# Kernel optimization log

Measured on AMD Instinct MI355X. Metric: run time of the kernel, lower is better.

The kernel has to match this reference:

```python
import jax, jax.numpy as jnp
import numpy as np
from jax.ops import segment_sum, segment_max

N, D, B = 1536, 32, 8            # nodes, candidate out-degree per node, sequential batch steps
OBS, HID, HEADS, C = 33, 64, 4, 8  # obs_dim, GRU hidden, attn heads, out_dim//heads
E = N * D


def setup_inputs() -> dict:
    key = jax.random.key(0)
    ks = jax.random.split(key, 16)
    g = lambda i, shape, s=0.1: jax.random.normal(ks[i], shape, jnp.float32) * s
    src = jnp.repeat(jnp.arange(N), D)                    # uniform degree -> scatter_topk = row top-k
    dst = jax.random.randint(ks[0], (E,), 0, N)
    return dict(
        H_t=jax.random.normal(ks[1], (B, N, OBS), jnp.float32),
        src=src, dst=dst, k=4,
        W_e1=g(2, (OBS, 32)), b_e1=jnp.zeros(32), W_e2=g(3, (32, 32)), b_e2=jnp.zeros(32),
        ln_g=jnp.ones(32), ln_b=jnp.zeros(32),
        W_ih=g(4, (3 * HID, 32)), W_hh=g(5, (3 * HID, HID)),
        b_ih=jnp.zeros(3 * HID), b_hh=jnp.zeros(3 * HID),
        W_s1=g(6, (2 * HID, 64)), b_s1=jnp.zeros(64), W_s2=g(7, (64, 1)), b_s2=jnp.zeros(1),
        W_gat=g(8, (HID, HEADS * C)), att_src=g(9, (HEADS, C)), att_dst=g(10, (HEADS, C)),
        b_gat=jnp.zeros(HEADS * C),
    )


def _layernorm(x, g, b, eps=1e-5):
    mu = x.mean(-1, keepdims=True)
    var = ((x - mu) ** 2).mean(-1, keepdims=True)
    return (x - mu) * jax.lax.rsqrt(var + eps) * g + b


def _forward(H_t, src, dst, k, W_e1, b_e1, W_e2, b_e2, ln_g, ln_b,
             W_ih, W_hh, b_ih, b_hh, W_s1, b_s1, W_s2, b_s2,
             W_gat, att_src, att_dst, b_gat):
    # ObsEmbedding: Linear-ReLU-Linear-ReLU-LayerNorm, applied to all (B,N) at once
    x = jax.nn.relu(H_t @ W_e1 + b_e1)
    x = jax.nn.relu(x @ W_e2 + b_e2)
    H_emb = _layernorm(x, ln_g, ln_b)              # (B,N,32)

    def step(h, e_t):
        # --- NodeMemory: shared GRUCell, h carried across batch steps ---
        gi = e_t @ W_ih.T + b_ih                   # (N,3H)
        gh = h @ W_hh.T + b_hh
        i_r, i_z, i_n = jnp.split(gi, 3, -1)
        h_r, h_z, h_n = jnp.split(gh, 3, -1)
        r = jax.nn.sigmoid(i_r + h_r)
        z = jax.nn.sigmoid(i_z + h_z)
        n = jnp.tanh(i_n + r * h_n)
        h_new = (1.0 - z) * n + z * h              # (N,HID)

        # --- EdgeScorer: sigmoid MLP score per candidate edge, keep top-k per source ---
        feat = jnp.concatenate([h_new[src], h_new[dst]], -1)        # (E,2*HID)
        score = jax.nn.sigmoid(
            (jax.nn.relu(feat @ W_s1 + b_s1) @ W_s2 + b_s2)[:, 0])  # (E,)
        s2 = score.reshape(N, D)
        top_idx = jax.lax.top_k(s2, k)[1]                           # (N,k)
        keep = (jnp.zeros((N, D), bool)
                .at[jnp.arange(N)[:, None], top_idx].set(True)).reshape(-1)  # (E,)
        w = jnp.where(keep, score, 0.0)                             # soft edge weights

        # --- GATConv (add_self_loops=False), pruned edges masked out of the softmax ---
        xh = (h_new @ W_gat).reshape(N, HEADS, C)
        a_s = (xh * att_src).sum(-1)               # (N,HEADS)
        a_d = (xh * att_dst).sum(-1)
        logit = jax.nn.leaky_relu(a_s[src] + a_d[dst], 0.2)         # (E,HEADS)
        logit = jnp.where(keep[:, None], logit, -1e30)
        m = segment_max(logit, dst, num_segments=N)                 # softmax grouped by target
        ex = jnp.where(keep[:, None], jnp.exp(logit - m[dst]), 0.0)
        ssum = segment_sum(ex, dst, num_segments=N)
        alpha = ex / jnp.clip(ssum[dst], 1e-16)                     # (E,HEADS)

        msg = alpha[:, :, None] * xh[src] * w[:, None, None]        # edge_weight scales messages
        out = segment_sum(msg, dst, num_segments=N).reshape(N, HEADS * C) + b_gat

        # --- densify attention: scatter-accumulate then row-normalize ---
        A = jnp.zeros((HEADS, N, N), alpha.dtype).at[:, src, dst].add(alpha.T)
        A = A / jnp.clip(A.sum(-1, keepdims=True), 1e-9)
        return h_new, (out, A)

    h0 = jnp.zeros((N, HID), H_t.dtype)
    _, (outs, attns) = jax.lax.scan(step, h0, H_emb)
    return outs, attns                              # (B,N,32), (B,HEADS,N,N)


def reference(H_t, src, dst, k, W_e1, b_e1, W_e2, b_e2, ln_g, ln_b,
              W_ih, W_hh, b_ih, b_hh, W_s1, b_s1, W_s2, b_s2,
              W_gat, att_src, att_dst, b_gat):
    return _forward(H_t, src, dst, k, W_e1, b_e1, W_e2, b_e2, ln_g, ln_b,
                    W_ih, W_hh, b_ih, b_hh, W_s1, b_s1, W_s2, b_s2,
                    W_gat, att_src, att_dst, b_gat)
```

## Files before the change

### kernel.cpp

```cpp
#include <hip/hip_runtime.h>
#include <math.h>

#define NN   1536
#define DG   32
#define BB   8
#define OBSD 33
#define HID  64
#define NHEAD 4
#define EE   (NN*DG)

__device__ __forceinline__ float sigm(float x){ return 1.0f/(1.0f+expf(-x)); }

__global__ void __launch_bounds__(256) k_embgi(
                      const float* __restrict__ Ht,
                      const float* __restrict__ We1, const float* __restrict__ be1,
                      const float* __restrict__ We2, const float* __restrict__ be2,
                      const float* __restrict__ lng, const float* __restrict__ lnb,
                      const float* __restrict__ Wih, const float* __restrict__ bih,
                      float* __restrict__ GI, int* __restrict__ cursor){
    __shared__ float lwih[192*33];
    int tid = threadIdx.x;
    if(blockIdx.x < 6) cursor[blockIdx.x*256 + tid] = 0;
    for(int i=tid;i<192*32;i+=256){ int r=i>>5, c=i&31; lwih[r*33+c]=Wih[i]; }
    __syncthreads();
    int lane = tid & 63;
    int j32 = lane & 31;
    int bn = blockIdx.x*4 + (tid>>6);
    const float* hrow = Ht + (size_t)bn*OBSD;
    float x1 = be1[j32];
    for(int o=0;o<OBSD;o++) x1 += hrow[o]*We1[o*32+j32];
    x1 = fmaxf(x1,0.f);
    float x2 = be2[j32];
    for(int i=0;i<32;i++){
        float xi = __shfl(x1, (lane & 32) | i, 64);
        x2 += xi * We2[i*32+j32];
    }
    x2 = fmaxf(x2,0.f);
    float mu = x2;
    for(int m=16;m>=1;m>>=1) mu += __shfl_xor(mu, m, 32);
    mu *= (1.0f/32.0f);
    float d = x2-mu; float var = d*d;
    for(int m=16;m>=1;m>>=1) var += __shfl_xor(var, m, 32);
    var *= (1.0f/32.0f);
    float xln = d*rsqrtf(var+1e-5f)*lng[j32]+lnb[j32];
    int j = lane;
    float gr=bih[j], gz=bih[64+j], gn=bih[128+j];
    for(int kk=0;kk<32;kk++){
        float ek = __shfl(xln, kk, 64);
        gr += ek*lwih[j*33+kk];
        gz += ek*lwih[(64+j)*33+kk];
        gn += ek*lwih[(128+j)*33+kk];
    }
    float* g = GI + (size_t)bn*192;
    g[j]=gr; g[64+j]=gz; g[128+j]=gn;
}

__global__ void k_count(const int* __restrict__ dst, int* __restrict__ cursor){
    int e = blockIdx.x*256+threadIdx.x;
    if(e<EE) atomicAdd(&cursor[dst[e]],1);
}
__global__ void k_scan(int* __restrict__ cnt, int* __restrict__ indptr){
    __shared__ int part[256];
    int t = threadIdx.x;
    int local[6]; int s=0;
    for(int i=0;i<6;i++){ local[i]=cnt[t*6+i]; s+=local[i]; }
    part[t]=s; __syncthreads();
    if(t==0){ int acc=0; for(int i=0;i<256;i++){ int v=part[i]; part[i]=acc; acc+=v; } }
    __syncthreads();
    int pre = part[t];
    for(int i=0;i<6;i++){ int idx=t*6+i; indptr[idx]=pre; cnt[idx]=pre; pre+=local[i]; }
    if(t==255) indptr[NN]=EE;
}
__global__ void k_fill(const int* __restrict__ dst, int* __restrict__ cursor, int* __restrict__ eids){
    int e = blockIdx.x*256+threadIdx.x;
    if(e<EE){ int p = atomicAdd(&cursor[dst[e]],1); eids[p]=e; }
}

__global__ void __launch_bounds__(384) k_gru_all(const float* __restrict__ GI,
                       const float* __restrict__ Whh, const float* __restrict__ bhh,
                       float* __restrict__ Hall){
    __shared__ float lw[192*65];
    int tid = threadIdx.x;
    for(int i=tid;i<192*64;i+=384){ int r=i>>6, c=i&63; lw[r*65+c]=Whh[i]; }
    __syncthreads();
    int node = blockIdx.x*6 + (tid>>6);
    int j = tid&63;
    float rw[64], rz[64], rn[64];
    #pragma unroll
    for(int kk=0;kk<64;kk++){
        rw[kk]=lw[j*65+kk];
        rz[kk]=lw[(64+j)*65+kk];
        rn[kk]=lw[(128+j)*65+kk];
    }
    float b_r=bhh[j], b_z=bhh[64+j], b_n=bhh[128+j];
    float hold = 0.f;
    for(int t=0;t<BB;t++){
        float hr=b_r, hz=b_z, hn=b_n;
        #pragma unroll
        for(int kk=0;kk<64;kk++){
            float hk = __shfl(hold,kk);
            hr += hk*rw[kk];
            hz += hk*rz[kk];
            hn += hk*rn[kk];
        }
        const float* g = GI + ((size_t)t*NN+node)*192;
        float r  = sigm(g[j]     + hr);
        float z  = sigm(g[64+j]  + hz);
        float nn_= tanhf(g[128+j] + r*hn);
        hold = (1.f-z)*nn_ + z*hold;
        Hall[((size_t)t*NN+node)*64 + j] = hold;
    }
}

__global__ void __launch_bounds__(256) k_post(const float* __restrict__ Hall,
                       const float* __restrict__ Ws1, const float* __restrict__ Wgat,
                       const float* __restrict__ atts, const float* __restrict__ attd,
                       float* __restrict__ P, float* __restrict__ Q,
                       float* __restrict__ xh, float* __restrict__ as_, float* __restrict__ ad_){
    __shared__ float ws1l[128*64];
    __shared__ float wgl[64*32];
    int tid = threadIdx.x;
    for(int i=tid;i<128*64;i+=256) ws1l[i]=Ws1[i];
    for(int i=tid;i<64*32;i+=256)  wgl[i]=Wgat[i];
    __syncthreads();
    int bn = blockIdx.x*4 + (tid>>6);
    int j = tid&63;
    float hv = Hall[(size_t)bn*64+j];
    float p=0.f,q=0.f,xv=0.f;
    for(int kk=0;kk<64;kk++){
        float hk=__shfl(hv,kk);
        p += hk*ws1l[kk*64+j];
        q += hk*ws1l[(64+kk)*64+j];
        if(j<32) xv += hk*wgl[kk*32+j];
    }
    P[(size_t)bn*64+j]=p; Q[(size_t)bn*64+j]=q;
    if(j<32){
        xh[(size_t)bn*32+j]=xv;
        float asv = xv*atts[j];
        float adv = xv*attd[j];
        for(int m=1;m<8;m<<=1){ asv += __shfl_xor(asv,m); adv += __shfl_xor(adv,m); }
        if((j&7)==0){ as_[(size_t)bn*4+(j>>3)]=asv; ad_[(size_t)bn*4+(j>>3)]=adv; }
    }
}

__global__ void __launch_bounds__(256) k_edge(const float* __restrict__ P, const float* __restrict__ Q,
                       const float* __restrict__ bs1, const float* __restrict__ Ws2,
                       const float* __restrict__ bs2, const int* __restrict__ dst,
                       const int* __restrict__ kptr, float* __restrict__ wbuf){
    __shared__ float sc[DG];
    int tid = threadIdx.x;
    int t = blockIdx.y;
    int row = blockIdx.x;
    int wv = tid>>6, j = tid&63;
    float pv = P[((size_t)t*NN+row)*64 + j];
    float bv = bs1[j], w2 = Ws2[j];
    float b2 = bs2[0];
    int des[8];
    #pragma unroll
    for(int i=0;i<8;i++) des[i] = dst[row*DG + wv*8 + i];
    float qv[8];
    #pragma unroll
    for(int i=0;i<8;i++) qv[i] = Q[((size_t)t*NN+des[i])*64 + j];
    #pragma unroll
    for(int i=0;i<8;i++){
        float v = fmaxf(pv+qv[i]+bv,0.f)*w2;
        for(int m=32;m>=1;m>>=1) v += __shfl_xor(v,m);
        if(j==0) sc[wv*8+i] = sigm(v+b2);
    }
    __syncthreads();
    if(tid<32){
        float score = sc[tid];
        int kk = kptr[0]; if(kk>32) kk=32; if(kk<0) kk=0;
        bool sel=false;
        for(int it=0; it<kk; it++){
            float v = sel ? -INFINITY : score;
            int idx = tid;
            for(int m=16;m>=1;m>>=1){
                float ov = __shfl_xor(v,m,32);
                int   oi = __shfl_xor(idx,m,32);
                if(ov>v || (ov==v && oi<idx)){ v=ov; idx=oi; }
            }
            if(idx==tid) sel=true;
        }
        wbuf[(size_t)t*EE + row*DG + tid] = sel ? score : 0.f;
    }
}

__global__ void __launch_bounds__(256) k_soft(const int* __restrict__ indptr, const int* __restrict__ eids,
                       const float* __restrict__ as_, const float* __restrict__ ad_,
                       const float* __restrict__ wbuf, const float* __restrict__ xhb,
                       const float* __restrict__ bgat,
                       float* __restrict__ alphab, float* __restrict__ outp){
    int n = blockIdx.x;
    int t = blockIdx.y;
    int h = threadIdx.x>>6;
    int lane = threadIdx.x&63;
    const float* w     = wbuf  + (size_t)t*EE;
    const float* asb   = as_   + (size_t)t*NN*4;
    const float* xhbt  = xhb   + (size_t)t*NN*32;
    float*       alpha = alphab+ (size_t)t*EE*4;
    int beg = indptr[n], end = indptr[n+1];
    int deg = end-beg;
    float adv = ad_[((size_t)t*NN+n)*4+h];
    float acc[8];
    #pragma unroll
    for(int c=0;c<8;c++) acc[c]=0.f;
    if(deg<=64){
        bool valid = lane<deg;
        int e = valid ? eids[beg+lane] : 0;
        float we = valid ? w[e] : 0.f;
        bool kept = we>0.f;
        int s = e>>5;
        float lg = -INFINITY, ex = 0.f;
        if(kept){
            lg = asb[s*4+h]+adv;
            lg = lg>0.f ? lg : 0.2f*lg;
        }
        float m = lg;
        for(int mm=32;mm>=1;mm>>=1) m = fmaxf(m,__shfl_xor(m,mm));
        if(kept) ex = expf(lg-m);
        float ssum = ex;
        for(int mm=32;mm>=1;mm>>=1) ssum += __shfl_xor(ssum,mm);
        float inv = 1.0f/fmaxf(ssum,1e-16f);
        if(kept){
            float a = ex*inv;
            alpha[e*4+h] = a;
            float aw = a*we;
            const float4* xr = (const float4*)(xhbt + s*32 + h*8);
            float4 x0 = xr[0], x1 = xr[1];
            acc[0]+=aw*x0.x; acc[1]+=aw*x0.y; acc[2]+=aw*x0.z; acc[3]+=aw*x0.w;
            acc[4]+=aw*x1.x; acc[5]+=aw*x1.y; acc[6]+=aw*x1.z; acc[7]+=aw*x1.w;
        }
    } else {
        float m = -INFINITY;
        for(int i=beg+lane;i<end;i+=64){
            int e = eids[i];
            if(w[e]>0.f){
                float lg = asb[(e>>5)*4+h]+adv;
                lg = lg>0.f ? lg : 0.2f*lg;
                m = fmaxf(m,lg);
            }
        }
        for(int mm=32;mm>=1;mm>>=1) m = fmaxf(m,__shfl_xor(m,mm));
        float ssum=0.f;
        for(int i=beg+lane;i<end;i+=64){
            int e = eids[i];
            float ex = 0.f;
            if(w[e]>0.f){
                float lg = asb[(e>>5)*4+h]+adv;
                lg = lg>0.f ? lg : 0.2f*lg;
                ex = expf(lg-m);
            }
            alpha[e*4+h]=ex;
            ssum += ex;
        }
        for(int mm=32;mm>=1;mm>>=1) ssum += __shfl_xor(ssum,mm);
        float inv = 1.0f/fmaxf(ssum,1e-16f);
        for(int i=beg+lane;i<end;i+=64){
            int e = eids[i];
            if(w[e]>0.f){
                float a = alpha[e*4+h]*inv;
                alpha[e*4+h]=a;
                float aw = a*w[e];
                const float* xr = xhbt + (e>>5)*32 + h*8;
                #pragma unroll
                for(int c=0;c<8;c++) acc[c] += aw*xr[c];
            } 
        }
    }
    for(int mm=32;mm>=1;mm>>=1){
        #pragma unroll
        for(int c=0;c<8;c++) acc[c] += __shfl_xor(acc[c],mm);
    }
    if(lane==0){
        float* o = outp + ((size_t)t*NN+n)*32 + h*8;
        float4 o0 = { acc[0]+bgat[h*8+0], acc[1]+bgat[h*8+1], acc[2]+bgat[h*8+2], acc[3]+bgat[h*8+3] };
        float4 o1 = { acc[4]+bgat[h*8+4], acc[5]+bgat[h*8+5], acc[6]+bgat[h*8+6], acc[7]+bgat[h*8+7] };
        ((float4*)o)[0]=o0; ((float4*)o)[1]=o1;
    }
}

__global__ void __launch_bounds__(256) k_scatter(const float* __restrict__ alphab,
                       const float* __restrict__ wbuf,
                       const int* __restrict__ dst, float* __restrict__ attn){
    __shared__ int   kde[DG];
    __shared__ float kan[DG][NHEAD];
    __shared__ int   scnt;
    int n = blockIdx.x;
    int t = blockIdx.y;
    int tid = threadIdx.x;
    const float* alpha = alphab + (size_t)t*EE*4;
    const float* w     = wbuf   + (size_t)t*EE;
    if(tid<64){
        int d = tid;
        int e = n*DG + d;
        bool kept = false;
        if(d<DG) kept = (w[e] > 0.f);
        unsigned long long mask = __ballot(kept);
        float4 av = {0.f,0.f,0.f,0.f};
        int de = 0;
        if(kept){ de = dst[e]; av = *(const float4*)(alpha + (size_t)e*4); }
        float s0=av.x, s1=av.y, s2=av.z, s3=av.w;
        for(int m=32;m>=1;m>>=1){
            s0 += __shfl_xor(s0,m); s1 += __shfl_xor(s1,m);
            s2 += __shfl_xor(s2,m); s3 += __shfl_xor(s3,m);
        }
        if(kept){
            int pos = __popcll(mask & ((1ull<<d)-1ull));
            kde[pos] = de;
            kan[pos][0] = av.x / fmaxf(s0,1e-9f);
            kan[pos][1] = av.y / fmaxf(s1,1e-9f);
            kan[pos][2] = av.z / fmaxf(s2,1e-9f);
            kan[pos][3] = av.w / fmaxf(s3,1e-9f);
        }
        if(tid==0) scnt = __popcll(mask);
    }
    __syncthreads();
    int cnt = scnt;
    size_t base = (size_t)t*NHEAD*NN*NN + (size_t)n*NN;
    #pragma unroll
    for(int it=0; it<6; it++){
        int c = it*256 + tid;
        int h = c/(NN/4), c4 = c%(NN/4);
        float4 f4 = {0.f,0.f,0.f,0.f};
        for(int p=0;p<cnt;p++){
            int de = kde[p];
            if((de>>2)==c4) ((float*)&f4)[de&3] += kan[p][h];
        }
        ((float4*)(attn + base + (size_t)h*NN*NN))[c4] = f4;
    }
}

extern "C" void kernel_launch(void* const* d_in, const int* in_sizes, int n_in,
                              void* d_out, int out_size, void* d_ws, size_t ws_size,
                              hipStream_t stream) {
    const float* Ht   = (const float*)d_in[0];
    const int*   dst  = (const int*)  d_in[2];
    const int*   kptr = (const int*)  d_in[3];
    const float* We1  = (const float*)d_in[4];
    const float* be1  = (const float*)d_in[5];
    const float* We2  = (const float*)d_in[6];
    const float* be2  = (const float*)d_in[7];
    const float* lng  = (const float*)d_in[8];
    const float* lnb  = (const float*)d_in[9];
    const float* Wih  = (const float*)d_in[10];
    const float* Whh  = (const float*)d_in[11];
    const float* bih  = (const float*)d_in[12];
    const float* bhh  = (const float*)d_in[13];
    const float* Ws1  = (const float*)d_in[14];
    const float* bs1  = (const float*)d_in[15];
    const float* Ws2  = (const float*)d_in[16];
    const float* bs2  = (const float*)d_in[17];
    const float* Wgat = (const float*)d_in[18];
    const float* atts = (const float*)d_in[19];
    const float* attd = (const float*)d_in[20];
    const float* bgat = (const float*)d_in[21];

    float* outp = (float*)d_out;
    float* attn = outp + (size_t)BB*NN*32;

    float* ws    = (float*)d_ws;
    float* GI    = ws;
    float* Hall  = ws + 2359296;
    float* P     = ws + 3145728;
    float* Q     = ws + 3932160;
    float* xh    = ws + 4718592;
    float* as_   = ws + 5111808;
    float* ad_   = ws + 5160960;
    float* wbuf  = ws + 5210112;
    float* alpha = ws + 5603328;
    int*   ibase = (int*)(ws + 7176192);
    int*   cursor= ibase;
    int*   indptr= ibase + 2048;
    int*   eids  = ibase + 4096;

    k_embgi<<<BB*NN/4, 256, 0, stream>>>(Ht, We1, be1, We2, be2, lng, lnb, Wih, bih, GI, cursor);
    k_count<<<EE/256, 256, 0, stream>>>(dst, cursor);
    k_scan<<<1, 256, 0, stream>>>(cursor, indptr);
    k_fill<<<EE/256, 256, 0, stream>>>(dst, cursor, eids);
    k_gru_all<<<NN/6, 384, 0, stream>>>(GI, Whh, bhh, Hall);
    k_post<<<BB*NN/4, 256, 0, stream>>>(Hall, Ws1, Wgat, atts, attd, P, Q, xh, as_, ad_);
    {
        dim3 g(NN, BB);
        k_edge<<<g, 256, 0, stream>>>(P, Q, bs1, Ws2, bs2, dst, kptr, wbuf);
        k_soft<<<g, 256, 0, stream>>>(indptr, eids, as_, ad_, wbuf, xh, bgat, alpha, outp);
        k_scatter<<<g, 256, 0, stream>>>(alpha, wbuf, dst, attn);
    }
}
```

Before: 544.3 us.

## Fuse GRU with post-projections and remap edge scorer to thread-per-edge

Merges the GRU recurrence kernel and the P/Q/xh/attention projection kernel, so each hidden state is projected right after it is produced and the Hall buffer round trip and one launch disappear. The GRU now reads recurrent weights from LDS each step instead of keeping 192 values per thread in registers, which lowers register pressure but adds LDS traffic. The edge scorer changes from one block per row with a wave-wide reduction per edge to one thread per edge looping over 64 features with float4 loads. That removes the shared memory and syncthreads but makes each thread read a full Q row. The fused kernel needs roughly 90KB of LDS per block, which limits occupancy with only 256 blocks.

```diff
diff --git a/kernel.cpp b/kernel.cpp
--- a/kernel.cpp
+++ b/kernel.cpp
@@ -76,70 +76,60 @@
     if(e<EE){ int p = atomicAdd(&cursor[dst[e]],1); eids[p]=e; }
 }
 
-__global__ void __launch_bounds__(384) k_gru_all(const float* __restrict__ GI,
+__global__ void __launch_bounds__(384) k_grupost(const float* __restrict__ GI,
                        const float* __restrict__ Whh, const float* __restrict__ bhh,
-                       float* __restrict__ Hall){
+                       const float* __restrict__ Ws1, const float* __restrict__ Wgat,
+                       const float* __restrict__ atts, const float* __restrict__ attd,
+                       float* __restrict__ P, float* __restrict__ Q,
+                       float* __restrict__ xh, float* __restrict__ as_, float* __restrict__ ad_){
     __shared__ float lw[192*65];
+    __shared__ float ws1l[128*64];
+    __shared__ float wgl[64*32];
     int tid = threadIdx.x;
     for(int i=tid;i<192*64;i+=384){ int r=i>>6, c=i&63; lw[r*65+c]=Whh[i]; }
+    for(int i=tid;i<128*64;i+=384) ws1l[i]=Ws1[i];
+    for(int i=tid;i<64*32;i+=384)  wgl[i]=Wgat[i];
     __syncthreads();
     int node = blockIdx.x*6 + (tid>>6);
     int j = tid&63;
-    float rw[64], rz[64], rn[64];
-    #pragma unroll
-    for(int kk=0;kk<64;kk++){
-        rw[kk]=lw[j*65+kk];
-        rz[kk]=lw[(64+j)*65+kk];
-        rn[kk]=lw[(128+j)*65+kk];
-    }
     float b_r=bhh[j], b_z=bhh[64+j], b_n=bhh[128+j];
+    const float* lwr = lw + j*65;
+    const float* lwz = lw + (64+j)*65;
+    const float* lwn = lw + (128+j)*65;
+    float atsv = (j<32)?atts[j]:0.f;
+    float atdv = (j<32)?attd[j]:0.f;
     float hold = 0.f;
     for(int t=0;t<BB;t++){
         float hr=b_r, hz=b_z, hn=b_n;
         #pragma unroll
         for(int kk=0;kk<64;kk++){
             float hk = __shfl(hold,kk);
-            hr += hk*rw[kk];
-            hz += hk*rz[kk];
-            hn += hk*rn[kk];
+            hr += hk*lwr[kk];
+            hz += hk*lwz[kk];
+            hn += hk*lwn[kk];
         }
         const float* g = GI + ((size_t)t*NN+node)*192;
         float r  = sigm(g[j]     + hr);
         float z  = sigm(g[64+j]  + hz);
         float nn_= tanhf(g[128+j] + r*hn);
         hold = (1.f-z)*nn_ + z*hold;
-        Hall[((size_t)t*NN+node)*64 + j] = hold;
-    }
-}
-
-__global__ void __launch_bounds__(256) k_post(const float* __restrict__ Hall,
-                       const float* __restrict__ Ws1, const float* __restrict__ Wgat,
-                       const float* __restrict__ atts, const float* __restrict__ attd,
-                       float* __restrict__ P, float* __restrict__ Q,
-                       float* __restrict__ xh, float* __restrict__ as_, float* __restrict__ ad_){
-    __shared__ float ws1l[128*64];
-    __shared__ float wgl[64*32];
-    int tid = threadIdx.x;
-    for(int i=tid;i<128*64;i+=256) ws1l[i]=Ws1[i];
-    for(int i=tid;i<64*32;i+=256)  wgl[i]=Wgat[i];
-    __syncthreads();
-    int bn = blockIdx.x*4 + (tid>>6);
-    int j = tid&63;
-    float hv = Hall[(size_t)bn*64+j];
-    float p=0.f,q=0.f,xv=0.f;
-    for(int kk=0;kk<64;kk++){
-        float hk=__shfl(hv,kk);
-        p += hk*ws1l[kk*64+j];
-        q += hk*ws1l[(64+kk)*64+j];
-        if(j<32) xv += hk*wgl[kk*32+j];
-    }
-    P[(size_t)bn*64+j]=p; Q[(size_t)bn*64+j]=q;
-    if(j<32){
-        xh[(size_t)bn*32+j]=xv;
-        float asv = xv*atts[j];
-        float adv = xv*attd[j];
-        for(int m=1;m<8;m<<=1){ asv += __shfl_xor(asv,m); adv += __shfl_xor(adv,m); }
-        if((j&7)==0){ as_[(size_t)bn*4+(j>>3)]=asv; ad_[(size_t)bn*4+(j>>3)]=adv; }
+        float p=0.f, q=0.f, xv=0.f;
+        #pragma unroll
+        for(int kk=0;kk<64;kk++){
+            float hk = __shfl(hold,kk);
+            p += hk*ws1l[kk*64+j];
+            q += hk*ws1l[(64+kk)*64+j];
+            if(j<32) xv += hk*wgl[kk*32+j];
+        }
+        size_t bn = (size_t)t*NN+node;
+        P[bn*64+j]=p; Q[bn*64+j]=q;
+        if(j<32){
+            xh[bn*32+j]=xv;
+            float asv = xv*atsv;
+            float adv = xv*atdv;
+            for(int m=1;m<8;m<<=1){ asv += __shfl_xor(asv,m); adv += __shfl_xor(adv,m); }
+            if((j&7)==0){ as_[bn*4+(j>>3)]=asv; ad_[bn*4+(j>>3)]=adv; }
+        }
     }
 }
 
@@ -147,43 +137,39 @@
                        const float* __restrict__ bs1, const float* __restrict__ Ws2,
                        const float* __restrict__ bs2, const int* __restrict__ dst,
                        const int* __restrict__ kptr, float* __restrict__ wbuf){
-    __shared__ float sc[DG];
     int tid = threadIdx.x;
     int t = blockIdx.y;
-    int row = blockIdx.x;
-    int wv = tid>>6, j = tid&63;
-    float pv = P[((size_t)t*NN+row)*64 + j];
-    float bv = bs1[j], w2 = Ws2[j];
-    float b2 = bs2[0];
-    int des[8];
+    int row = blockIdx.x*8 + (tid>>5);
+    int d = tid & 31;
+    int e = row*DG + d;
+    int de = dst[e];
+    const float4* Pr = (const float4*)(P + ((size_t)t*NN+row)*64);
+    const float4* Qr = (const float4*)(Q + ((size_t)t*NN+de)*64);
+    const float4* B1 = (const float4*)bs1;
+    const float4* W2 = (const float4*)Ws2;
+    float acc = 0.f;
     #pragma unroll
-    for(int i=0;i<8;i++) des[i] = dst[row*DG + wv*8 + i];
-    float qv[8];
-    #pragma unroll
-    for(int i=0;i<8;i++) qv[i] = Q[((size_t)t*NN+des[i])*64 + j];
-    #pragma unroll
-    for(int i=0;i<8;i++){
-        float v = fmaxf(pv+qv[i]+bv,0.f)*w2;
-        for(int m=32;m>=1;m>>=1) v += __shfl_xor(v,m);
-        if(j==0) sc[wv*8+i] = sigm(v+b2);
-    }
-    __syncthreads();
-    if(tid<32){
-        float score = sc[tid];
-        int kk = kptr[0]; if(kk>32) kk=32; if(kk<0) kk=0;
-        bool sel=false;
-        for(int it=0; it<kk; it++){
-            float v = sel ? -INFINITY : score;
-            int idx = tid;
-            for(int m=16;m>=1;m>>=1){
-                float ov = __shfl_xor(v,m,32);
-                int   oi = __shfl_xor(idx,m,32);
-                if(ov>v || (ov==v && oi<idx)){ v=ov; idx=oi; }
-            }
-            if(idx==tid) sel=true;
-        }
-        wbuf[(size_t)t*EE + row*DG + tid] = sel ? score : 0.f;
-    }
+    for(int jj=0;jj<16;jj++){
+        float4 pv=Pr[jj], qv=Qr[jj], bv=B1[jj], wv=W2[jj];
+        acc += fmaxf(pv.x+qv.x+bv.x,0.f)*wv.x;
+        acc += fmaxf(pv.y+qv.y+bv.y,0.f)*wv.y;
+        acc += fmaxf(pv.z+qv.z+bv.z,0.f)*wv.z;
+        acc += fmaxf(pv.w+qv.w+bv.w,0.f)*wv.w;
+    }
+    float score = sigm(acc + bs2[0]);
+    int kk = kptr[0]; if(kk>32) kk=32; if(kk<0) kk=0;
+    bool sel=false;
+    for(int it=0; it<kk; it++){
+        float v = sel ? -INFINITY : score;
+        int idx = d;
+        for(int m=16;m>=1;m>>=1){
+            float ov = __shfl_xor(v,m,32);
+            int   oi = __shfl_xor(idx,m,32);
+            if(ov>v || (ov==v && oi<idx)){ v=ov; idx=oi; }
+        }
+        if(idx==d) sel=true;
+    }
+    wbuf[(size_t)t*EE + e] = sel ? score : 0.f;
 }
 
 __global__ void __launch_bounds__(256) k_soft(const int* __restrict__ indptr, const int* __restrict__ eids,
@@ -265,7 +251,7 @@
                 const float* xr = xhbt + (e>>5)*32 + h*8;
                 #pragma unroll
                 for(int c=0;c<8;c++) acc[c] += aw*xr[c];
-            } 
+            }
         }
     }
     for(int mm=32;mm>=1;mm>>=1){
@@ -361,15 +347,14 @@
 
     float* ws    = (float*)d_ws;
     float* GI    = ws;
-    float* Hall  = ws + 2359296;
-    float* P     = ws + 3145728;
-    float* Q     = ws + 3932160;
-    float* xh    = ws + 4718592;
-    float* as_   = ws + 5111808;
-    float* ad_   = ws + 5160960;
-    float* wbuf  = ws + 5210112;
-    float* alpha = ws + 5603328;
-    int*   ibase = (int*)(ws + 7176192);
+    float* P     = ws + 2359296;
+    float* Q     = ws + 3145728;
+    float* xh    = ws + 3932160;
+    float* as_   = ws + 4325376;
+    float* ad_   = ws + 4374528;
+    float* wbuf  = ws + 4423680;
+    float* alpha = ws + 4816896;
+    int*   ibase = (int*)(ws + 6389760);
     int*   cursor= ibase;
     int*   indptr= ibase + 2048;
     int*   eids  = ibase + 4096;
@@ -378,11 +363,11 @@
     k_count<<<EE/256, 256, 0, stream>>>(dst, cursor);
     k_scan<<<1, 256, 0, stream>>>(cursor, indptr);
     k_fill<<<EE/256, 256, 0, stream>>>(dst, cursor, eids);
-    k_gru_all<<<NN/6, 384, 0, stream>>>(GI, Whh, bhh, Hall);
-    k_post<<<BB*NN/4, 256, 0, stream>>>(Hall, Ws1, Wgat, atts, attd, P, Q, xh, as_, ad_);
+    k_grupost<<<NN/6, 384, 0, stream>>>(GI, Whh, bhh, Ws1, Wgat, atts, attd, P, Q, xh, as_, ad_);
     {
+        dim3 ge(NN/8, BB);
+        k_edge<<<ge, 256, 0, stream>>>(P, Q, bs1, Ws2, bs2, dst, kptr, wbuf);
         dim3 g(NN, BB);
-        k_edge<<<g, 256, 0, stream>>>(P, Q, bs1, Ws2, bs2, dst, kptr, wbuf);
         k_soft<<<g, 256, 0, stream>>>(indptr, eids, as_, ad_, wbuf, xh, bgat, alpha, outp);
         k_scatter<<<g, 256, 0, stream>>>(alpha, wbuf, dst, attn);
     }
```

Measured after the change: 738.0 us. +35.6%, slower.
